# Performance work log

Hardware: AMD Instinct MI355X
Metric: run time of the kernel (lower is better)

The kernel has to match this reference:

```python
import jax, jax.numpy as jnp
import numpy as np

B, L, C, H, O = 2048, 128, 32, 64, 16
N_SUB = 2  # fixed RK4 substeps per knot interval (stands in for torchdiffeq adaptive solver)


def hermite_coeffs(x, t):
    """torchcde.hermite_cubic_coefficients_with_backward_differences.
    x: (B, L, D), t: (L,) -> coeffs (B, L-1, 4*D) packed [a, b, 2c, 3d]."""
    dt = (t[1:] - t[:-1])[None, :, None]            # (1, L-1, 1)
    secants = (x[:, 1:] - x[:, :-1]) / dt           # (B, L-1, D)
    derivs = jnp.concatenate([secants[:, :1], secants], axis=1)  # backward diffs, first repeated
    x0, x1 = x[:, :-1], x[:, 1:]
    d0, d1 = derivs[:, :-1], derivs[:, 1:]
    delta = x1 - x0
    a = x0
    b = d0
    two_c = 2.0 * (3.0 * delta / dt - 2.0 * d0 - d1) / dt
    three_d = 3.0 * (-2.0 * delta / dt + d0 + d1) / (dt * dt)
    return jnp.concatenate([a, b, two_c, three_d], axis=-1)


def setup_inputs() -> dict:
    key = jax.random.key(0)
    ks = jax.random.split(key, 8)
    t = jnp.arange(L, dtype=jnp.float32)
    # coherent random control path -> spline coeffs (as torchcde would produce)
    path = jnp.cumsum(jax.random.normal(ks[0], (B, L, C), jnp.float32) * 0.1, axis=1)
    coeffs = hermite_coeffs(path, t)
    def lin(k, fan_in, fan_out):
        return jax.random.normal(k, (fan_in, fan_out), jnp.float32) / np.float32(np.sqrt(fan_in))
    return {
        "coeffs": coeffs,
        "t": t,
        "W_init": lin(ks[1], C, H), "b_init": jnp.zeros((H,), jnp.float32),
        "W1": lin(ks[2], H, 2), "b1": jnp.zeros((2,), jnp.float32),
        "W2": lin(ks[3], 2, H * C), "b2": jnp.zeros((H * C,), jnp.float32),
        "W_read": lin(ks[4], H, O), "b_read": jnp.zeros((O,), jnp.float32),
    }


def reference(coeffs, t, W_init, b_init, W1, b1, W2, b2, W_read, b_read):
    a, b, two_c, three_d = jnp.split(coeffs, 4, axis=-1)  # each (B, L-1, C)

    # X(interval[0]) = a of first interval
    X0 = a[:, 0]                                   # (B, C)
    z0 = X0 @ W_init + b_init                      # (B, H); dropout p=0 is a no-op

    def f(z):  # CDEFunc: (B,H) -> (B,H,C)
        h1 = jax.nn.relu(z @ W1 + b1)
        g = jnp.tanh(h1 @ W2 + b2)
        return g.reshape(z.shape[0], H, C)

    def g(z, bi, ci, di, s):  # f(z) @ dX/dt(s)
        dXdt = bi + ci * s + di * (s * s)          # (B, C)
        return jnp.einsum('bhc,bc->bh', f(z), dXdt)

    def interval_step(z, xs):
        bi, ci, di, dti = xs
        hstep = dti / N_SUB
        def sub(z, j):
            s = j * hstep
            k1 = g(z, bi, ci, di, s)
            k2 = g(z + 0.5 * hstep * k1, bi, ci, di, s + 0.5 * hstep)
            k3 = g(z + 0.5 * hstep * k2, bi, ci, di, s + 0.5 * hstep)
            k4 = g(z + hstep * k3, bi, ci, di, s + hstep)
            z = z + (hstep / 6.0) * (k1 + 2.0 * k2 + 2.0 * k3 + k4)
            return z, None
        z, _ = jax.lax.scan(sub, z, jnp.arange(N_SUB, dtype=jnp.float32))
        return z, z

    dt = t[1:] - t[:-1]                            # (L-1,)
    xs = (jnp.moveaxis(b, 1, 0), jnp.moveaxis(two_c, 1, 0), jnp.moveaxis(three_d, 1, 0), dt)
    _, z_seq = jax.lax.scan(interval_step, z0, xs)  # (L-1, B, H)

    z_T = jnp.moveaxis(jnp.concatenate([z0[None], z_seq], axis=0), 0, 1)  # (B, L, H)
    z_T = jnp.tanh(z_T)
    pred_y = z_T @ W_read + b_read                 # (B, L, O)
    new_coeffs = hermite_coeffs(pred_y, t)         # (B, L-1, 4*O)
    return pred_y, new_coeffs
```

## Files before the change

kernel.cpp:

```cpp
#include <hip/hip_runtime.h>
#include <cstdint>
#include <cstddef>

constexpr int Bn = 2048, Ln = 128, Cn = 32, Hn = 64, On = 16;
constexpr int NIv = Ln - 1;
constexpr float K2 = 2.885390081777927f;

__device__ __forceinline__ float fexp2(float x) {
#if __has_builtin(__builtin_amdgcn_exp2f)
  return __builtin_amdgcn_exp2f(x);
#else
  float r; asm("v_exp_f32 %0, %1" : "=v"(r) : "v"(x)); return r;
#endif
}
__device__ __forceinline__ float frcpf(float x) {
#if __has_builtin(__builtin_amdgcn_rcpf)
  return __builtin_amdgcn_rcpf(x);
#else
  float r; asm("v_rcp_f32 %0, %1" : "=v"(r) : "v"(x)); return r;
#endif
}
__device__ __forceinline__ float tanh_fast(float x) {
  float e = fexp2(K2 * x);
  return fmaf(-2.0f, frcpf(e + 1.0f), 1.0f);
}

__global__ __launch_bounds__(256, 2) void ncde_scan_kernel(
    const float* __restrict__ coeffs, const float* __restrict__ t,
    const float* __restrict__ W_init, const float* __restrict__ b_init,
    const float* __restrict__ W1, const float* __restrict__ b1,
    const float* __restrict__ W2, const float* __restrict__ b2,
    float* __restrict__ zt)
{
  __shared__ float sdx[4][5][32];
  const int wv = threadIdx.x >> 6;
  const int lane = threadIdx.x & 63;
  const int b = (blockIdx.x << 2) | wv;

  const float w10 = W1[2 * lane], w11 = W1[2 * lane + 1];
  const float sb0 = b1[0], sb1 = b1[1];
  float w20[32], w21[32], bb[32];
  {
    const float* W2a = W2 + lane * 32;
    const float* W2b = W2 + 2048 + lane * 32;
    const float* b2a = b2 + lane * 32;
#pragma unroll
    for (int c4 = 0; c4 < 8; ++c4) {
      float4 x0 = *(const float4*)(W2a + 4 * c4);
      float4 x1 = *(const float4*)(W2b + 4 * c4);
      float4 x2 = *(const float4*)(b2a + 4 * c4);
      w20[4*c4+0] = x0.x*K2; w20[4*c4+1] = x0.y*K2; w20[4*c4+2] = x0.z*K2; w20[4*c4+3] = x0.w*K2;
      w21[4*c4+0] = x1.x*K2; w21[4*c4+1] = x1.y*K2; w21[4*c4+2] = x1.z*K2; w21[4*c4+3] = x1.w*K2;
      bb [4*c4+0] = x2.x*K2; bb [4*c4+1] = x2.y*K2; bb [4*c4+2] = x2.z*K2; bb [4*c4+3] = x2.w*K2;
    }
  }

  const float* cb0 = coeffs + (size_t)b * NIv * 128;
  if (lane < 32) sdx[wv][0][lane] = cb0[lane];
  __builtin_amdgcn_wave_barrier();
  float z = b_init[lane];
#pragma unroll 4
  for (int c = 0; c < 32; ++c)
    z = fmaf(sdx[wv][0][c], W_init[(c << 6) + lane], z);
  zt[(size_t)b * Ln * Hn + lane] = tanh_fast(z);

  for (int i = 0; i < NIv; ++i) {
    const float* cb = cb0 + (size_t)i * 128;
    const float dti = t[i + 1] - t[i];
    const float hst = 0.5f * dti;
    __builtin_amdgcn_wave_barrier();
    if (lane < 32) {
      const float bi = cb[32 + lane];
      const float ci = cb[64 + lane];
      const float di = cb[96 + lane];
      const float q = 0.25f * dti;
#pragma unroll
      for (int k = 0; k < 5; ++k) {
        const float s = q * (float)k;
        sdx[wv][k][lane] = fmaf(fmaf(di, s, ci), s, bi);
      }
    }
    __builtin_amdgcn_wave_barrier();

#pragma unroll 1
    for (int j = 0; j < 2; ++j) {
      float kacc = 0.0f, kprev = 0.0f;
#pragma unroll
      for (int st = 0; st < 4; ++st) {
        const float cin = (st == 0) ? 0.0f : (st == 3) ? hst : 0.5f * hst;
        const float wgt = (st == 1 || st == 2) ? 2.0f : 1.0f;
        const float* dx = &sdx[wv][2 * j + ((st + 1) >> 1)][0];
        const float zs = fmaf(cin, kprev, z);
        float p0 = zs * w10, p1 = zs * w11;
#pragma unroll
        for (int m = 1; m < 64; m <<= 1) {
          p0 += __shfl_xor(p0, m, 64);
          p1 += __shfl_xor(p1, m, 64);
        }
        const float h10 = fmaxf(p0 + sb0, 0.0f);
        const float h11 = fmaxf(p1 + sb1, 0.0f);
        float acc = 0.0f;
#pragma unroll
        for (int c4 = 0; c4 < 8; ++c4) {
          const float4 d4 = *(const float4*)(dx + 4 * c4);
          const float dv0 = d4.x, dv1 = d4.y, dv2 = d4.z, dv3 = d4.w;
#pragma unroll
          for (int q2 = 0; q2 < 4; ++q2) {
            const int c = 4 * c4 + q2;
            const float u = fmaf(h10, w20[c], fmaf(h11, w21[c], bb[c]));
            const float e = fexp2(u);
            const float r = frcpf(e + 1.0f);
            const float th = fmaf(-2.0f, r, 1.0f);
            const float dvq = (q2 == 0) ? dv0 : (q2 == 1) ? dv1 : (q2 == 2) ? dv2 : dv3;
            acc = fmaf(th, dvq, acc);
          }
        }
        kprev = acc;
        kacc = fmaf(wgt, acc, kacc);
      }
      z = fmaf(hst * (1.0f / 6.0f), kacc, z);
    }
    zt[((size_t)b * Ln + (i + 1)) * Hn + lane] = tanh_fast(z);
  }
}

#define SPX(l_, o_) (((l_) << 4) | (((o_) + (l_)) & 15))
#define SZX(l_, h_) (((l_) << 6) | (((h_) + (l_)) & 63))

__global__ __launch_bounds__(128, 2) void ncde_epilogue_kernel(
    const float* __restrict__ zt, const float* __restrict__ t,
    const float* __restrict__ W_read, const float* __restrict__ b_read,
    float* __restrict__ out)
{
  __shared__ float sW[Hn * On];
  __shared__ float sz[Ln * Hn];
  __shared__ float sp[Ln * On];
  __shared__ float st_[Ln];
  const int b = blockIdx.x;
  const int tid = threadIdx.x;

  for (int i2 = tid; i2 < Hn * On; i2 += 128) sW[i2] = W_read[i2];
  st_[tid] = t[tid];
  const float* zb = zt + (size_t)b * Ln * Hn;
#pragma unroll 1
  for (int r = 0; r < 16; ++r) {
    const int base = (r * 128 + tid) * 4;
    const float4 v = *(const float4*)(zb + base);
    const int l = base >> 6, h = base & 63;
    sz[SZX(l, h + 0)] = v.x;
    sz[SZX(l, h + 1)] = v.y;
    sz[SZX(l, h + 2)] = v.z;
    sz[SZX(l, h + 3)] = v.w;
  }
  __syncthreads();

  float acc0[On];
#pragma unroll
  for (int o = 0; o < On; ++o) acc0[o] = b_read[o];
#pragma unroll 2
  for (int h = 0; h < Hn; ++h) {
    const float zv = sz[SZX(tid, h)];
#pragma unroll
    for (int o = 0; o < On; ++o) acc0[o] = fmaf(zv, sW[h * On + o], acc0[o]);
  }
  float* po = out + ((size_t)b * Ln + tid) * On;
#pragma unroll
  for (int o = 0; o < On; ++o) sp[SPX(tid, o)] = acc0[o];
#pragma unroll
  for (int o4 = 0; o4 < 4; ++o4) {
    float4 v = make_float4(acc0[4*o4], acc0[4*o4+1], acc0[4*o4+2], acc0[4*o4+3]);
    *(float4*)(po + 4 * o4) = v;
  }
  __syncthreads();

  float* cbo = out + (size_t)Bn * Ln * On + (size_t)b * NIv * 64;
#pragma unroll 1
  for (int r = 0; r < 16; ++r) {
    const int item = r * 128 + tid;
    if (item < NIv * On) {
      const int i = item >> 4, o = item & 15;
      const float p0 = sp[SPX(i, o)], p1 = sp[SPX(i + 1, o)];
      const float rdt = frcpf(st_[i + 1] - st_[i]);
      const float si = (p1 - p0) * rdt;
      float d0;
      if (i == 0) d0 = si;
      else d0 = (p0 - sp[SPX(i - 1, o)]) * frcpf(st_[i] - st_[i - 1]);
      const float d1 = si;
      float* cc = cbo + (size_t)i * 64 + o;
      cc[0]  = p0;
      cc[16] = d0;
      cc[32] = 2.0f * (3.0f * si - 2.0f * d0 - d1) * rdt;
      cc[48] = 3.0f * (d0 + d1 - 2.0f * si) * (rdt * rdt);
    }
  }
}

extern "C" void kernel_launch(void* const* d_in, const int* in_sizes, int n_in,
                              void* d_out, int out_size, void* d_ws, size_t ws_size,
                              hipStream_t stream) {
  const float* coeffs = (const float*)d_in[0];
  const float* t      = (const float*)d_in[1];
  const float* W_init = (const float*)d_in[2];
  const float* b_init = (const float*)d_in[3];
  const float* W1     = (const float*)d_in[4];
  const float* b1     = (const float*)d_in[5];
  const float* W2     = (const float*)d_in[6];
  const float* b2     = (const float*)d_in[7];
  const float* W_read = (const float*)d_in[8];
  const float* b_read = (const float*)d_in[9];
  float* out = (float*)d_out;
  float* zt  = (float*)d_ws;

  ncde_scan_kernel<<<dim3(Bn / 4), dim3(256), 0, stream>>>(
      coeffs, t, W_init, b_init, W1, b1, W2, b2, zt);
  ncde_epilogue_kernel<<<dim3(Bn), dim3(128), 0, stream>>>(
      zt, t, W_read, b_read, out);
}
```

Measured before the change: 1.491 ms.

## Use DPP/readlane reductions and packed FMA in NCDE scan inner loop

Swaps the shuffle-xor butterfly reduction of z·W1 for DPP row sums plus four readlanes. Computes the W2 pre-activations with v_pk_fma_f32 on paired registers and splits the tanh-dot accumulator into four independent chains. It also unrolls the two RK4 substeps so the scheduler can see across them. The goal is lower latency on the serial per-stage critical path, at the cost of inline asm and more register pressure.

```diff
diff --git a/kernel.cpp b/kernel.cpp
--- a/kernel.cpp
+++ b/kernel.cpp
@@ -5,6 +5,8 @@
 constexpr int Bn = 2048, Ln = 128, Cn = 32, Hn = 64, On = 16;
 constexpr int NIv = Ln - 1;
 constexpr float K2 = 2.885390081777927f;
+
+typedef float v2f __attribute__((ext_vector_type(2)));
 
 __device__ __forceinline__ float fexp2(float x) {
 #if __has_builtin(__builtin_amdgcn_exp2f)
@@ -24,6 +26,34 @@
   float e = fexp2(K2 * x);
   return fmaf(-2.0f, frcpf(e + 1.0f), 1.0f);
 }
+
+__device__ __forceinline__ v2f pk_fma(v2f a, v2f b, v2f c) {
+  v2f d;
+  asm("v_pk_fma_f32 %0, %1, %2, %3" : "=v"(d) : "v"(a), "v"(b), "v"(c));
+  return d;
+}
+
+template<int CTRL>
+__device__ __forceinline__ float dpp_addstep(float p) {
+  int q = __builtin_amdgcn_update_dpp(0, __float_as_int(p), CTRL, 0xF, 0xF, true);
+  return p + __int_as_float(q);
+}
+__device__ __forceinline__ float dpp_rowsum16(float p) {
+  p = dpp_addstep<0xB1>(p);
+  p = dpp_addstep<0x4E>(p);
+  p = dpp_addstep<0x141>(p);
+  p = dpp_addstep<0x140>(p);
+  return p;
+}
+__device__ __forceinline__ float lane4_total(float p) {
+  float s0 = __int_as_float(__builtin_amdgcn_readlane(__float_as_int(p), 0));
+  float s1 = __int_as_float(__builtin_amdgcn_readlane(__float_as_int(p), 16));
+  float s2 = __int_as_float(__builtin_amdgcn_readlane(__float_as_int(p), 32));
+  float s3 = __int_as_float(__builtin_amdgcn_readlane(__float_as_int(p), 48));
+  return (s0 + s1) + (s2 + s3);
+}
+
+#define REP8(M) M(0) M(1) M(2) M(3) M(4) M(5) M(6) M(7)
 
 __global__ __launch_bounds__(256, 2) void ncde_scan_kernel(
     const float* __restrict__ coeffs, const float* __restrict__ t,
@@ -36,34 +66,37 @@
   const int wv = threadIdx.x >> 6;
   const int lane = threadIdx.x & 63;
   const int b = (blockIdx.x << 2) | wv;
+  float* const sdxw = &sdx[wv][0][0];
 
   const float w10 = W1[2 * lane], w11 = W1[2 * lane + 1];
   const float sb0 = b1[0], sb1 = b1[1];
-  float w20[32], w21[32], bb[32];
+
+#define DECLW(g) v2f w20a##g, w20b##g, w21a##g, w21b##g, ba##g, bb##g;
+  REP8(DECLW)
   {
     const float* W2a = W2 + lane * 32;
     const float* W2b = W2 + 2048 + lane * 32;
     const float* b2a = b2 + lane * 32;
-#pragma unroll
-    for (int c4 = 0; c4 < 8; ++c4) {
-      float4 x0 = *(const float4*)(W2a + 4 * c4);
-      float4 x1 = *(const float4*)(W2b + 4 * c4);
-      float4 x2 = *(const float4*)(b2a + 4 * c4);
-      w20[4*c4+0] = x0.x*K2; w20[4*c4+1] = x0.y*K2; w20[4*c4+2] = x0.z*K2; w20[4*c4+3] = x0.w*K2;
-      w21[4*c4+0] = x1.x*K2; w21[4*c4+1] = x1.y*K2; w21[4*c4+2] = x1.z*K2; w21[4*c4+3] = x1.w*K2;
-      bb [4*c4+0] = x2.x*K2; bb [4*c4+1] = x2.y*K2; bb [4*c4+2] = x2.z*K2; bb [4*c4+3] = x2.w*K2;
-    }
+#define LOADW(g) { \
+      const float4 x0 = *(const float4*)(W2a + 4 * (g)); \
+      const float4 x1 = *(const float4*)(W2b + 4 * (g)); \
+      const float4 x2 = *(const float4*)(b2a + 4 * (g)); \
+      w20a##g = (v2f){x0.x * K2, x0.y * K2}; w20b##g = (v2f){x0.z * K2, x0.w * K2}; \
+      w21a##g = (v2f){x1.x * K2, x1.y * K2}; w21b##g = (v2f){x1.z * K2, x1.w * K2}; \
+      ba##g   = (v2f){x2.x * K2, x2.y * K2}; bb##g   = (v2f){x2.z * K2, x2.w * K2}; }
+    REP8(LOADW)
   }
 
   const float* cb0 = coeffs + (size_t)b * NIv * 128;
-  if (lane < 32) sdx[wv][0][lane] = cb0[lane];
+  if (lane < 32) sdxw[lane] = cb0[lane];
   __builtin_amdgcn_wave_barrier();
   float z = b_init[lane];
 #pragma unroll 4
   for (int c = 0; c < 32; ++c)
-    z = fmaf(sdx[wv][0][c], W_init[(c << 6) + lane], z);
+    z = fmaf(sdxw[c], W_init[(c << 6) + lane], z);
   zt[(size_t)b * Ln * Hn + lane] = tanh_fast(z);
 
+#pragma unroll 1
   for (int i = 0; i < NIv; ++i) {
     const float* cb = cb0 + (size_t)i * 128;
     const float dti = t[i + 1] - t[i];
@@ -77,49 +110,48 @@
 #pragma unroll
       for (int k = 0; k < 5; ++k) {
         const float s = q * (float)k;
-        sdx[wv][k][lane] = fmaf(fmaf(di, s, ci), s, bi);
+        sdxw[k * 32 + lane] = fmaf(fmaf(di, s, ci), s, bi);
       }
     }
     __builtin_amdgcn_wave_barrier();
 
-#pragma unroll 1
+    float kacc = 0.0f, kprev = 0.0f;
+#pragma unroll
     for (int j = 0; j < 2; ++j) {
-      float kacc = 0.0f, kprev = 0.0f;
+      if (j == 1) { z = fmaf(hst * (1.0f / 6.0f), kacc, z); kacc = 0.0f; kprev = 0.0f; }
 #pragma unroll
       for (int st = 0; st < 4; ++st) {
         const float cin = (st == 0) ? 0.0f : (st == 3) ? hst : 0.5f * hst;
         const float wgt = (st == 1 || st == 2) ? 2.0f : 1.0f;
-        const float* dx = &sdx[wv][2 * j + ((st + 1) >> 1)][0];
+        const int kidx = 2 * j + ((st + 1) >> 1);
+        const float* dx = sdxw + kidx * 32;
         const float zs = fmaf(cin, kprev, z);
-        float p0 = zs * w10, p1 = zs * w11;
-#pragma unroll
-        for (int m = 1; m < 64; m <<= 1) {
-          p0 += __shfl_xor(p0, m, 64);
-          p1 += __shfl_xor(p1, m, 64);
-        }
-        const float h10 = fmaxf(p0 + sb0, 0.0f);
-        const float h11 = fmaxf(p1 + sb1, 0.0f);
-        float acc = 0.0f;
-#pragma unroll
-        for (int c4 = 0; c4 < 8; ++c4) {
-          const float4 d4 = *(const float4*)(dx + 4 * c4);
-          const float dv0 = d4.x, dv1 = d4.y, dv2 = d4.z, dv3 = d4.w;
-#pragma unroll
-          for (int q2 = 0; q2 < 4; ++q2) {
-            const int c = 4 * c4 + q2;
-            const float u = fmaf(h10, w20[c], fmaf(h11, w21[c], bb[c]));
-            const float e = fexp2(u);
-            const float r = frcpf(e + 1.0f);
-            const float th = fmaf(-2.0f, r, 1.0f);
-            const float dvq = (q2 == 0) ? dv0 : (q2 == 1) ? dv1 : (q2 == 2) ? dv2 : dv3;
-            acc = fmaf(th, dvq, acc);
-          }
-        }
+        float p0 = dpp_rowsum16(zs * w10);
+        float p1 = dpp_rowsum16(zs * w11);
+        const float h10 = fmaxf(lane4_total(p0) + sb0, 0.0f);
+        const float h11 = fmaxf(lane4_total(p1) + sb1, 0.0f);
+        const v2f hb0 = (v2f){h10, h10};
+        const v2f hb1 = (v2f){h11, h11};
+        float a0 = 0.0f, a1 = 0.0f, a2 = 0.0f, a3 = 0.0f;
+#define GRP(g) { \
+        const float4 d4 = *(const float4*)(dx + 4 * (g)); \
+        const v2f u0 = pk_fma(w20a##g, hb0, pk_fma(w21a##g, hb1, ba##g)); \
+        const v2f u1 = pk_fma(w20b##g, hb0, pk_fma(w21b##g, hb1, bb##g)); \
+        const float e0 = fexp2(u0.x), e1 = fexp2(u0.y); \
+        const float e2 = fexp2(u1.x), e3 = fexp2(u1.y); \
+        const float r0 = frcpf(e0 + 1.0f), r1 = frcpf(e1 + 1.0f); \
+        const float r2 = frcpf(e2 + 1.0f), r3 = frcpf(e3 + 1.0f); \
+        a0 = fmaf(fmaf(-2.0f, r0, 1.0f), d4.x, a0); \
+        a1 = fmaf(fmaf(-2.0f, r1, 1.0f), d4.y, a1); \
+        a2 = fmaf(fmaf(-2.0f, r2, 1.0f), d4.z, a2); \
+        a3 = fmaf(fmaf(-2.0f, r3, 1.0f), d4.w, a3); }
+        REP8(GRP)
+        const float acc = (a0 + a1) + (a2 + a3);
         kprev = acc;
         kacc = fmaf(wgt, acc, kacc);
       }
-      z = fmaf(hst * (1.0f / 6.0f), kacc, z);
     }
+    z = fmaf(hst * (1.0f / 6.0f), kacc, z);
     zt[((size_t)b * Ln + (i + 1)) * Hn + lane] = tanh_fast(z);
   }
 }
```

Measured after the change: 1.305 ms. 1.14x faster.
